# Optimization experiments

Measured on AMD Instinct MI355X. Metric: run time of the kernel, lower is better.

Reference implementation:

```python
import jax, jax.numpy as jnp
import numpy as np

IN_DIM = 64
OUT_DIM = 64
NUM_HEADS = 4
NEG_SLOPE = 0.2
GAMMA = 1.0  # constraint_gamma
NUM_VARS = 100000
NUM_CLAUSES = 100000
NUM_CLUSTERS = 2048
VARS_PER = 64
CLAUSES_PER = 64
NUM_EDGES = 400000


def _xavier(k, shape):
    bound = np.sqrt(6.0 / (shape[0] + shape[1])).astype(np.float32)
    return jax.random.uniform(k, shape, jnp.float32, -bound, bound)


def setup_inputs() -> dict:
    key = jax.random.key(0)
    ks = jax.random.split(key, 11)
    return {
        "x_var": jax.random.normal(ks[0], (NUM_VARS, IN_DIM), jnp.float32),
        "x_clause": jax.random.normal(ks[1], (NUM_CLAUSES, IN_DIM), jnp.float32),
        "var_clause_edge_index": jax.random.randint(ks[2], (2, NUM_EDGES), 0, NUM_VARS),
        "edge_polarity": jax.random.normal(ks[3], (NUM_EDGES, 1), jnp.float32),
        "cluster_var_ids": jax.random.randint(ks[4], (NUM_CLUSTERS, VARS_PER), 0, NUM_VARS),
        "cluster_clause_ids": jax.random.randint(ks[5], (NUM_CLUSTERS, CLAUSES_PER), 0, NUM_CLAUSES),
        "satisfaction_scores": jax.random.uniform(ks[6], (NUM_CLAUSES,), jnp.float32),
        "active_heads": 4,
        "W_Q": _xavier(ks[7], (OUT_DIM, IN_DIM)),
        "W_K": _xavier(ks[8], (OUT_DIM, IN_DIM)),
        "W_V": _xavier(ks[9], (OUT_DIM, IN_DIM)),
        "head_weights": jnp.ones((NUM_HEADS,), jnp.float32),
        "out_proj_w": _xavier(ks[10], (OUT_DIM, OUT_DIM)),
        "out_proj_b": jnp.zeros((OUT_DIM,), jnp.float32),
    }


def reference(x_var, x_clause, var_clause_edge_index, edge_polarity,
              cluster_var_ids, cluster_clause_ids, satisfaction_scores,
              active_heads, W_Q, W_K, W_V, head_weights, out_proj_w, out_proj_b):
    # NOTE: var_clause_edge_index / edge_polarity are accepted but unused,
    # matching the original forward body.
    num_vars = x_var.shape[0]
    x_all = jnp.concatenate([x_var, x_clause], axis=0)            # [N, D]
    Q = x_all @ W_Q.T
    K = x_all @ W_K.T
    V = x_all @ W_V.T

    # Block-diagonal cluster layout: [C, S] with S = VARS_PER + CLAUSES_PER
    nodes = jnp.concatenate([cluster_var_ids, cluster_clause_ids + num_vars], axis=1)
    Qc = Q[nodes]                                                 # [C, S, D]
    Kc = K[nodes]
    Vc = V[nodes]

    scale = jnp.asarray(np.sqrt(OUT_DIM), Qc.dtype)
    scores = jnp.einsum('csd,ctd->cst', Qc, Kc) / scale            # [C, S, S]
    # constraint-aware bias on clause columns (added before leaky_relu)
    bias = jnp.concatenate(
        [jnp.zeros(cluster_var_ids.shape, scores.dtype),
         GAMMA * satisfaction_scores[cluster_clause_ids]], axis=1)  # [C, S]
    scores = jax.nn.leaky_relu(scores + bias[:, None, :], NEG_SLOPE)
    attn = jax.nn.softmax(scores, axis=-1)

    head_w = jnp.mean(head_weights[:active_heads])
    h = jnp.einsum('cst,ctd->csd', attn, Vc) * head_w             # [C, S, D]

    flat = nodes.reshape(-1)
    out = jnp.zeros_like(x_all).at[flat].add(h.reshape(-1, OUT_DIM))
    count = jnp.zeros((x_all.shape[0],), x_all.dtype).at[flat].add(1.0)
    out = out / jnp.maximum(count, 1.0)[:, None]
    out = out @ out_proj_w.T + out_proj_b

    return (x_var + out[:num_vars], x_clause + out[num_vars:])
```

## Files before the change

kernel.cpp:

```cpp
#include <hip/hip_runtime.h>


#define NV 100000
#define NN 200000
#define NCLUST 2048
#define XS 72

typedef __attribute__((ext_vector_type(8))) short short8;
typedef __attribute__((ext_vector_type(16))) float floatx16;
typedef __attribute__((ext_vector_type(4))) unsigned uint4v;

__device__ __forceinline__ unsigned short f2bf(float f) {
    union { float f; unsigned u; } v; v.f = f;
    unsigned r = v.u + 0x7fffu + ((v.u >> 16) & 1u);
    return (unsigned short)(r >> 16);
}
__device__ __forceinline__ unsigned pack2bf(float lo, float hi) {
    union { float f; unsigned u; } a, b; a.f = lo; b.f = hi;
    unsigned ra = a.u + 0x7fffu + ((a.u >> 16) & 1u);
    unsigned rb = b.u + 0x7fffu + ((b.u >> 16) & 1u);
    return (ra >> 16) | (rb & 0xffff0000u);
}
__device__ __forceinline__ int crow(int r, int lane) {
    return (r & 3) + 8 * (r >> 2) + 4 * (lane >> 5);
}
__device__ __forceinline__ void bar_lds() {
    __builtin_amdgcn_sched_barrier(0);
    asm volatile("s_waitcnt lgkmcnt(0)" ::: "memory");
    __builtin_amdgcn_s_barrier();
    __builtin_amdgcn_sched_barrier(0);
}

#define ZU4 1600000
__global__ __launch_bounds__(256) void prep_kernel(
    const float* __restrict__ WQ, const float* __restrict__ WK,
    const float* __restrict__ WV, const float* __restrict__ Wout,
    const float* __restrict__ head_weights, const int* __restrict__ active_heads_p,
    const int* __restrict__ cvar, const int* __restrict__ ccl,
    unsigned short* __restrict__ Mtr, unsigned short* __restrict__ Pbf,
    uint4v* __restrict__ zbase, float* __restrict__ countv)
{
    int o = blockIdx.x * blockDim.x + threadIdx.x;
    if (o < 4096) {
        int d = o >> 6, a = o & 63;
        float acc = 0.f;
        for (int j = 0; j < 64; ++j) acc += WQ[j*64 + a] * WK[j*64 + d];
        Mtr[o] = f2bf(acc * 0.125f);
    } else if (o < 8192) {
        int ah = active_heads_p[0];
        float hw = 0.f;
        for (int i = 0; i < ah; ++i) hw += head_weights[i];
        hw /= (float)ah;
        int o2 = o - 4096;
        int j = o2 >> 6, b = o2 & 63;
        float acc = 0.f;
        for (int d = 0; d < 64; ++d) acc += Wout[j*64 + d] * WV[d*64 + b];
        Pbf[o2] = f2bf(acc * hw);
    }
    {
        int c = o >> 7, r = o & 127;
        int nid = (r < 64) ? cvar[c * 64 + r] : (NV + ccl[c * 64 + (r - 64)]);
        atomicAdd(&countv[nid], 1.0f);
    }
    uint4v z = {0u, 0u, 0u, 0u};
    for (int j = o; j < ZU4; j += 262144) zbase[j] = z;
}

template<bool WN>
__device__ __forceinline__ void cluster_compute(
    unsigned short* X, unsigned short* E,
    const int* ids, const float* biascl,
    const unsigned short* __restrict__ Mtr,
    unsigned short* __restrict__ accum_bf,
    int lane, int w, int m, int hk, int r, int cb,
    short8 nx0, short8 nx1, short8 nx2, short8 nx3)
{
    {
        floatx16 z0 = {}, z1 = {};
        #pragma unroll
        for (int ks = 0; ks < 4; ++ks) {
            short8 mb0 = *(const short8*)(Mtr + m * 64 + ks * 16 + hk);
            short8 mb1 = *(const short8*)(Mtr + (32 + m) * 64 + ks * 16 + hk);
            short8 a = *(const short8*)&X[(w * 32 + m) * XS + ks * 16 + hk];
            z0 = __builtin_amdgcn_mfma_f32_32x32x16_bf16(a, mb0, z0, 0, 0, 0);
            z1 = __builtin_amdgcn_mfma_f32_32x32x16_bf16(a, mb1, z1, 0, 0, 0);
        }
        #pragma unroll
        for (int rr = 0; rr < 16; ++rr) {
            int row = w * 32 + crow(rr, lane);
            E[row * XS + m]      = f2bf(z0[rr]);
            E[row * XS + 32 + m] = f2bf(z1[rr]);
        }
    }

    floatx16 sc[4] = {{}, {}, {}, {}};
    #pragma unroll
    for (int ks = 0; ks < 4; ++ks) {
        short8 a = *(const short8*)&E[(w * 32 + m) * XS + ks * 16 + hk];
        #pragma unroll
        for (int nt = 0; nt < 4; ++nt) {
            short8 b = *(const short8*)&X[(nt * 32 + m) * XS + ks * 16 + hk];
            sc[nt] = __builtin_amdgcn_mfma_f32_32x32x16_bf16(a, b, sc[nt], 0, 0, 0);
        }
    }

    const float b2 = biascl[m], b3 = biascl[32 + m];
    #pragma unroll
    for (int rr = 0; rr < 16; ++rr) {
        float a0 = sc[0][rr], a1 = sc[1][rr], a2 = sc[2][rr] + b2, a3 = sc[3][rr] + b3;
        a0 = a0 > 0.f ? a0 : 0.2f * a0;
        a1 = a1 > 0.f ? a1 : 0.2f * a1;
        a2 = a2 > 0.f ? a2 : 0.2f * a2;
        a3 = a3 > 0.f ? a3 : 0.2f * a3;
        a0 = __expf(a0); a1 = __expf(a1); a2 = __expf(a2); a3 = __expf(a3);
        float s4 = (a0 + a1) + (a2 + a3);
        #pragma unroll
        for (int off = 1; off < 32; off <<= 1) s4 += __shfl_xor(s4, off, 64);
        float inv = __builtin_amdgcn_rcpf(s4);
        sc[0][rr] = a0 * inv; sc[1][rr] = a1 * inv;
        sc[2][rr] = a2 * inv; sc[3][rr] = a3 * inv;
    }

    #pragma unroll
    for (int rr = 0; rr < 16; ++rr) {
        int row = w * 32 + crow(rr, lane);
        E[row * XS + m]      = f2bf(sc[0][rr]);
        E[row * XS + 32 + m] = f2bf(sc[1][rr]);
    }

    floatx16 g0 = {}, g1 = {};
    #pragma unroll
    for (int ks = 0; ks < 4; ++ks) {
        short8 a = *(const short8*)&E[(w * 32 + m) * XS + ks * 16 + hk];
        short8 b0, b1;
        #pragma unroll
        for (int j = 0; j < 8; ++j) {
            int t = ks * 16 + hk + j;
            b0[j] = (short)X[t * XS + m];
            b1[j] = (short)X[t * XS + 32 + m];
        }
        g0 = __builtin_amdgcn_mfma_f32_32x32x16_bf16(a, b0, g0, 0, 0, 0);
        g1 = __builtin_amdgcn_mfma_f32_32x32x16_bf16(a, b1, g1, 0, 0, 0);
    }

    #pragma unroll
    for (int rr = 0; rr < 16; ++rr) {
        int row = w * 32 + crow(rr, lane);
        E[row * XS + m]      = f2bf(sc[2][rr]);
        E[row * XS + 32 + m] = f2bf(sc[3][rr]);
    }

    #pragma unroll
    for (int ks = 0; ks < 4; ++ks) {
        short8 a = *(const short8*)&E[(w * 32 + m) * XS + ks * 16 + hk];
        short8 b0, b1;
        #pragma unroll
        for (int j = 0; j < 8; ++j) {
            int t = 64 + ks * 16 + hk + j;
            b0[j] = (short)X[t * XS + m];
            b1[j] = (short)X[t * XS + 32 + m];
        }
        g0 = __builtin_amdgcn_mfma_f32_32x32x16_bf16(a, b0, g0, 0, 0, 0);
        g1 = __builtin_amdgcn_mfma_f32_32x32x16_bf16(a, b1, g1, 0, 0, 0);
    }

    if (WN) {
        *(short8*)&E[r * XS + cb +  0] = nx0;
        *(short8*)&E[r * XS + cb +  8] = nx1;
        *(short8*)&E[r * XS + cb + 16] = nx2;
        *(short8*)&E[r * XS + cb + 24] = nx3;
    }

    const bool ev = !(lane & 1);
    const int colbase = ev ? m : (31 + m);
    #pragma unroll
    for (int rr = 0; rr < 16; ++rr) {
        int row = w * 32 + crow(rr, lane);
        int nid = ids[row];
        float a0 = g0[rr], a1 = g1[rr];
        float t0 = __shfl_xor(a0, 1, 64);
        float t1 = __shfl_xor(a1, 1, 64);
        float lo = ev ? a0 : t1;
        float hi = ev ? t0 : a1;
        unsigned pk = (unsigned)f2bf(lo) | ((unsigned)f2bf(hi) << 16);
        unsigned long long addr =
            (unsigned long long)(accum_bf + (size_t)nid * 64 + colbase);
        asm volatile("global_atomic_pk_add_bf16 %0, %1, off"
                     :: "v"(addr), "v"(pk) : "memory");
    }
}

__global__ __launch_bounds__(256, 4) void attn_kernel(
    const float* __restrict__ x_var, const float* __restrict__ x_clause,
    const int* __restrict__ cvar, const int* __restrict__ ccl,
    const float* __restrict__ sat, const unsigned short* __restrict__ Mtr,
    unsigned short* __restrict__ accum_bf)
{
    __shared__ unsigned short bufA[128 * XS];
    __shared__ unsigned short bufB[128 * XS];
    __shared__ int   ids0[128], ids1[128];
    __shared__ float bias0[64], bias1[64];

    const int tid = threadIdx.x, lane = tid & 63, w = tid >> 6;
    const int m = lane & 31, hk = (lane >> 5) * 8;
    const int c0 = blockIdx.x * 2;
    const int r = tid >> 1, half = tid & 1, cb = half * 32;

    int nid0, nid1;
    const float *src0, *src1;
    float sv0 = 0.f, sv1 = 0.f;
    if (r < 64) {
        nid0 = cvar[c0 * 64 + r];
        nid1 = cvar[c0 * 64 + 64 + r];
        src0 = x_var + (size_t)nid0 * 64;
        src1 = x_var + (size_t)nid1 * 64;
    } else {
        int cid0 = ccl[c0 * 64 + (r - 64)];
        int cid1 = ccl[c0 * 64 + r];
        nid0 = NV + cid0; nid1 = NV + cid1;
        src0 = x_clause + (size_t)cid0 * 64;
        src1 = x_clause + (size_t)cid1 * 64;
        if (half) { sv0 = sat[cid0]; sv1 = sat[cid1]; }
    }

    const float4* s40 = (const float4*)src0 + half * 8;
    const float4* s41 = (const float4*)src1 + half * 8;
    float4 v0[8], v1[8];
    #pragma unroll
    for (int i = 0; i < 8; ++i) v0[i] = s40[i];
    #pragma unroll
    for (int i = 0; i < 8; ++i) v1[i] = s41[i];

    if (!half) { ids0[r] = nid0; ids1[r] = nid1; }
    if (r >= 64 && half) { bias0[r - 64] = sv0; bias1[r - 64] = sv1; }

    {
        union { unsigned u[16]; short8 v[4]; } h0;
        #pragma unroll
        for (int i = 0; i < 8; ++i) {
            h0.u[2*i]   = pack2bf(v0[i].x, v0[i].y);
            h0.u[2*i+1] = pack2bf(v0[i].z, v0[i].w);
        }
        #pragma unroll
        for (int i = 0; i < 4; ++i) *(short8*)&bufA[r * XS + cb + i * 8] = h0.v[i];
    }
    union { unsigned u[16]; short8 v[4]; } h1;
    #pragma unroll
    for (int i = 0; i < 8; ++i) {
        h1.u[2*i]   = pack2bf(v1[i].x, v1[i].y);
        h1.u[2*i+1] = pack2bf(v1[i].z, v1[i].w);
    }

    bar_lds();

    cluster_compute<true>(bufA, bufB, ids0, bias0, Mtr, accum_bf,
                          lane, w, m, hk, r, cb,
                          h1.v[0], h1.v[1], h1.v[2], h1.v[3]);

    bar_lds();

    short8 zz = {};
    cluster_compute<false>(bufB, bufA, ids1, bias1, Mtr, accum_bf,
                           lane, w, m, hk, r, cb, zz, zz, zz, zz);
}

__global__ __launch_bounds__(256, 4) void finalize_kernel(
    const float* __restrict__ x_var, const float* __restrict__ x_clause,
    const unsigned short* __restrict__ accum_bf, const float* __restrict__ countv,
    const unsigned short* __restrict__ Pbf, const float* __restrict__ bout,
    float* __restrict__ out)
{
    __shared__ float T[4][32][68];
    __shared__ float cnts[256];
    const int tid = threadIdx.x, lane = tid & 63, w = tid >> 6;
    const int base = blockIdx.x * 256;
    {
        int n = base + tid;
        cnts[tid] = (n < NN) ? countv[n] : 1.f;
    }
    __syncthreads();

    const int m = lane & 31, hk = (lane >> 5) * 8;
    short8 pb[2][4];
    #pragma unroll
    for (int nt = 0; nt < 2; ++nt)
        #pragma unroll
        for (int ks = 0; ks < 4; ++ks)
            pb[nt][ks] = *(const short8*)(Pbf + (nt * 32 + m) * 64 + ks * 16 + hk);
    const float bias0 = bout[m], bias1 = bout[32 + m];

    const int r2 = lane >> 1, cb2 = (lane & 1) * 32;

    #pragma unroll
    for (int tm = 0; tm < 2; ++tm) {
        int mt = w * 2 + tm;
        const unsigned short* arow = accum_bf + (size_t)(base + mt * 32 + m) * 64;
        floatx16 c0 = {}, c1 = {};
        #pragma unroll
        for (int ks = 0; ks < 4; ++ks) {
            short8 a = *(const short8*)(arow + ks * 16 + hk);
            c0 = __builtin_amdgcn_mfma_f32_32x32x16_bf16(a, pb[0][ks], c0, 0, 0, 0);
            c1 = __builtin_amdgcn_mfma_f32_32x32x16_bf16(a, pb[1][ks], c1, 0, 0, 0);
        }
        #pragma unroll
        for (int rr = 0; rr < 16; ++rr) {
            int lr32 = crow(rr, lane);
            float inv = 1.0f / fmaxf(cnts[mt * 32 + lr32], 1.0f);
            T[w][lr32][m]      = c0[rr] * inv + bias0;
            T[w][lr32][32 + m] = c1[rr] * inv + bias1;
        }
        int n2 = base + mt * 32 + r2;
        if (n2 < NN) {
            const float* xr = (n2 < NV) ? (x_var + (size_t)n2 * 64)
                                        : (x_clause + (size_t)(n2 - NV) * 64);
            float* orow = out + (size_t)n2 * 64;
            #pragma unroll
            for (int j = 0; j < 8; ++j) {
                float4 t = *(const float4*)&T[w][r2][cb2 + 4 * j];
                float4 xv = *(const float4*)&xr[cb2 + 4 * j];
                float4 o;
                o.x = t.x + xv.x; o.y = t.y + xv.y;
                o.z = t.z + xv.z; o.w = t.w + xv.w;
                *(float4*)&orow[cb2 + 4 * j] = o;
            }
        }
    }
}

extern "C" void kernel_launch(void* const* d_in, const int* in_sizes, int n_in,
                              void* d_out, int out_size, void* d_ws, size_t ws_size,
                              hipStream_t stream)
{
    const float* x_var        = (const float*)d_in[0];
    const float* x_clause     = (const float*)d_in[1];
    const int*   cvar         = (const int*)d_in[4];
    const int*   ccl          = (const int*)d_in[5];
    const float* sat          = (const float*)d_in[6];
    const int*   active_heads = (const int*)d_in[7];
    const float* WQ           = (const float*)d_in[8];
    const float* WK           = (const float*)d_in[9];
    const float* WV           = (const float*)d_in[10];
    const float* head_weights = (const float*)d_in[11];
    const float* Wout         = (const float*)d_in[12];
    const float* bout         = (const float*)d_in[13];

    unsigned short* accum_bf = (unsigned short*)d_ws;
    float* countv = (float*)(accum_bf + (size_t)NN * 64);
    unsigned short* Mtr = (unsigned short*)(countv + NN);
    unsigned short* Pbf = Mtr + 4096;

    hipMemsetAsync(countv, 0, (size_t)NN * 4, stream);
    prep_kernel<<<1024, 256, 0, stream>>>(WQ, WK, WV, Wout, head_weights,
                                          active_heads, cvar, ccl, Mtr, Pbf,
                                          (uint4v*)d_ws, countv);
    attn_kernel<<<NCLUST / 2, 256, 0, stream>>>(
        x_var, x_clause, cvar, ccl, sat, Mtr, accum_bf);
    finalize_kernel<<<(NN + 255) / 256, 256, 0, stream>>>(
        x_var, x_clause, accum_bf, countv, Pbf, bout, (float*)d_out);
}
```

Measured before the change: 216.4 us.

## Fuse prep, attention and finalize into one persistent kernel with grid barriers

Replaces the three separate kernel launches with one kernel of 1024 blocks. The blocks move through a zeroing and weight-prep phase, a count-atomics phase, the attention phase and the finalize phase, with software grid barriers between phases. Shared memory is reused across phases through a raw buffer cast to per-phase structs. The aim is to remove launch gaps and tail effects between kernels. In exchange it adds three spin-wait grid barriers. It also relies on all 1024 blocks being co-resident; if they are not, the barriers can deadlock.

```diff
diff --git a/kernel.cpp b/kernel.cpp
--- a/kernel.cpp
+++ b/kernel.cpp
@@ -5,6 +5,7 @@
 #define NN 200000
 #define NCLUST 2048
 #define XS 72
+#define GRIDN 1024
 
 typedef __attribute__((ext_vector_type(8))) short short8;
 typedef __attribute__((ext_vector_type(16))) float floatx16;
@@ -30,41 +31,29 @@
     __builtin_amdgcn_s_barrier();
     __builtin_amdgcn_sched_barrier(0);
 }
-
-#define ZU4 1600000
-__global__ __launch_bounds__(256) void prep_kernel(
-    const float* __restrict__ WQ, const float* __restrict__ WK,
-    const float* __restrict__ WV, const float* __restrict__ Wout,
-    const float* __restrict__ head_weights, const int* __restrict__ active_heads_p,
-    const int* __restrict__ cvar, const int* __restrict__ ccl,
-    unsigned short* __restrict__ Mtr, unsigned short* __restrict__ Pbf,
-    uint4v* __restrict__ zbase, float* __restrict__ countv)
-{
-    int o = blockIdx.x * blockDim.x + threadIdx.x;
-    if (o < 4096) {
-        int d = o >> 6, a = o & 63;
-        float acc = 0.f;
-        for (int j = 0; j < 64; ++j) acc += WQ[j*64 + a] * WK[j*64 + d];
-        Mtr[o] = f2bf(acc * 0.125f);
-    } else if (o < 8192) {
-        int ah = active_heads_p[0];
-        float hw = 0.f;
-        for (int i = 0; i < ah; ++i) hw += head_weights[i];
-        hw /= (float)ah;
-        int o2 = o - 4096;
-        int j = o2 >> 6, b = o2 & 63;
-        float acc = 0.f;
-        for (int d = 0; d < 64; ++d) acc += Wout[j*64 + d] * WV[d*64 + b];
-        Pbf[o2] = f2bf(acc * hw);
-    }
-    {
-        int c = o >> 7, r = o & 127;
-        int nid = (r < 64) ? cvar[c * 64 + r] : (NV + ccl[c * 64 + (r - 64)]);
-        atomicAdd(&countv[nid], 1.0f);
-    }
-    uint4v z = {0u, 0u, 0u, 0u};
-    for (int j = o; j < ZU4; j += 262144) zbase[j] = z;
-}
+__device__ __forceinline__ void grid_bar(int* ctr) {
+    __syncthreads();
+    if (threadIdx.x == 0) {
+        __hip_atomic_fetch_add(ctr, 1, __ATOMIC_ACQ_REL, __HIP_MEMORY_SCOPE_AGENT);
+        int v;
+        do {
+            __builtin_amdgcn_s_sleep(2);
+            v = __hip_atomic_load(ctr, __ATOMIC_ACQUIRE, __HIP_MEMORY_SCOPE_AGENT);
+        } while (v < GRIDN);
+    }
+    __syncthreads();
+}
+
+struct SmemAttn {
+    unsigned short bufA[128 * XS];
+    unsigned short bufB[128 * XS];
+    int ids0[128], ids1[128];
+    float bias0[64], bias1[64];
+};
+struct SmemFin {
+    float T[4][32][68];
+    float cnts[256];
+};
 
 template<bool WN>
 __device__ __forceinline__ void cluster_compute(
@@ -190,138 +179,173 @@
     }
 }
 
-__global__ __launch_bounds__(256, 4) void attn_kernel(
+extern "C" __global__ __launch_bounds__(256, 4) void fused_kernel(
     const float* __restrict__ x_var, const float* __restrict__ x_clause,
     const int* __restrict__ cvar, const int* __restrict__ ccl,
-    const float* __restrict__ sat, const unsigned short* __restrict__ Mtr,
-    unsigned short* __restrict__ accum_bf)
-{
-    __shared__ unsigned short bufA[128 * XS];
-    __shared__ unsigned short bufB[128 * XS];
-    __shared__ int   ids0[128], ids1[128];
-    __shared__ float bias0[64], bias1[64];
-
-    const int tid = threadIdx.x, lane = tid & 63, w = tid >> 6;
-    const int m = lane & 31, hk = (lane >> 5) * 8;
-    const int c0 = blockIdx.x * 2;
-    const int r = tid >> 1, half = tid & 1, cb = half * 32;
-
-    int nid0, nid1;
-    const float *src0, *src1;
-    float sv0 = 0.f, sv1 = 0.f;
-    if (r < 64) {
-        nid0 = cvar[c0 * 64 + r];
-        nid1 = cvar[c0 * 64 + 64 + r];
-        src0 = x_var + (size_t)nid0 * 64;
-        src1 = x_var + (size_t)nid1 * 64;
-    } else {
-        int cid0 = ccl[c0 * 64 + (r - 64)];
-        int cid1 = ccl[c0 * 64 + r];
-        nid0 = NV + cid0; nid1 = NV + cid1;
-        src0 = x_clause + (size_t)cid0 * 64;
-        src1 = x_clause + (size_t)cid1 * 64;
-        if (half) { sv0 = sat[cid0]; sv1 = sat[cid1]; }
-    }
-
-    const float4* s40 = (const float4*)src0 + half * 8;
-    const float4* s41 = (const float4*)src1 + half * 8;
-    float4 v0[8], v1[8];
-    #pragma unroll
-    for (int i = 0; i < 8; ++i) v0[i] = s40[i];
-    #pragma unroll
-    for (int i = 0; i < 8; ++i) v1[i] = s41[i];
-
-    if (!half) { ids0[r] = nid0; ids1[r] = nid1; }
-    if (r >= 64 && half) { bias0[r - 64] = sv0; bias1[r - 64] = sv1; }
-
-    {
-        union { unsigned u[16]; short8 v[4]; } h0;
-        #pragma unroll
-        for (int i = 0; i < 8; ++i) {
-            h0.u[2*i]   = pack2bf(v0[i].x, v0[i].y);
-            h0.u[2*i+1] = pack2bf(v0[i].z, v0[i].w);
-        }
-        #pragma unroll
-        for (int i = 0; i < 4; ++i) *(short8*)&bufA[r * XS + cb + i * 8] = h0.v[i];
-    }
-    union { unsigned u[16]; short8 v[4]; } h1;
-    #pragma unroll
-    for (int i = 0; i < 8; ++i) {
-        h1.u[2*i]   = pack2bf(v1[i].x, v1[i].y);
-        h1.u[2*i+1] = pack2bf(v1[i].z, v1[i].w);
-    }
-
-    bar_lds();
-
-    cluster_compute<true>(bufA, bufB, ids0, bias0, Mtr, accum_bf,
-                          lane, w, m, hk, r, cb,
-                          h1.v[0], h1.v[1], h1.v[2], h1.v[3]);
-
-    bar_lds();
-
-    short8 zz = {};
-    cluster_compute<false>(bufB, bufA, ids1, bias1, Mtr, accum_bf,
-                           lane, w, m, hk, r, cb, zz, zz, zz, zz);
-}
-
-__global__ __launch_bounds__(256, 4) void finalize_kernel(
-    const float* __restrict__ x_var, const float* __restrict__ x_clause,
-    const unsigned short* __restrict__ accum_bf, const float* __restrict__ countv,
-    const unsigned short* __restrict__ Pbf, const float* __restrict__ bout,
+    const float* __restrict__ sat,
+    const float* __restrict__ WQ, const float* __restrict__ WK,
+    const float* __restrict__ WV, const float* __restrict__ Wout,
+    const float* __restrict__ head_weights, const int* __restrict__ active_heads_p,
+    const float* __restrict__ bout,
+    unsigned short* __restrict__ accum_bf, float* __restrict__ countv,
+    int* __restrict__ barp,
+    unsigned short* __restrict__ Mtr, unsigned short* __restrict__ Pbf,
     float* __restrict__ out)
 {
-    __shared__ float T[4][32][68];
-    __shared__ float cnts[256];
-    const int tid = threadIdx.x, lane = tid & 63, w = tid >> 6;
-    const int base = blockIdx.x * 256;
+    __shared__ __align__(16) char smem_raw[sizeof(SmemAttn)];
+
+    const int tid = threadIdx.x, bid = blockIdx.x;
+    const int gthread = bid * 256 + tid;
+    const int lane = tid & 63, w = tid >> 6;
+    const int m = lane & 31, hk = (lane >> 5) * 8;
+
     {
-        int n = base + tid;
-        cnts[tid] = (n < NN) ? countv[n] : 1.f;
-    }
-    __syncthreads();
-
-    const int m = lane & 31, hk = (lane >> 5) * 8;
-    short8 pb[2][4];
-    #pragma unroll
-    for (int nt = 0; nt < 2; ++nt)
-        #pragma unroll
-        for (int ks = 0; ks < 4; ++ks)
-            pb[nt][ks] = *(const short8*)(Pbf + (nt * 32 + m) * 64 + ks * 16 + hk);
-    const float bias0 = bout[m], bias1 = bout[32 + m];
-
-    const int r2 = lane >> 1, cb2 = (lane & 1) * 32;
-
-    #pragma unroll
-    for (int tm = 0; tm < 2; ++tm) {
-        int mt = w * 2 + tm;
-        const unsigned short* arow = accum_bf + (size_t)(base + mt * 32 + m) * 64;
-        floatx16 c0 = {}, c1 = {};
-        #pragma unroll
-        for (int ks = 0; ks < 4; ++ks) {
-            short8 a = *(const short8*)(arow + ks * 16 + hk);
-            c0 = __builtin_amdgcn_mfma_f32_32x32x16_bf16(a, pb[0][ks], c0, 0, 0, 0);
-            c1 = __builtin_amdgcn_mfma_f32_32x32x16_bf16(a, pb[1][ks], c1, 0, 0, 0);
-        }
-        #pragma unroll
-        for (int rr = 0; rr < 16; ++rr) {
-            int lr32 = crow(rr, lane);
-            float inv = 1.0f / fmaxf(cnts[mt * 32 + lr32], 1.0f);
-            T[w][lr32][m]      = c0[rr] * inv + bias0;
-            T[w][lr32][32 + m] = c1[rr] * inv + bias1;
-        }
-        int n2 = base + mt * 32 + r2;
-        if (n2 < NN) {
-            const float* xr = (n2 < NV) ? (x_var + (size_t)n2 * 64)
-                                        : (x_clause + (size_t)(n2 - NV) * 64);
-            float* orow = out + (size_t)n2 * 64;
-            #pragma unroll
-            for (int j = 0; j < 8; ++j) {
-                float4 t = *(const float4*)&T[w][r2][cb2 + 4 * j];
-                float4 xv = *(const float4*)&xr[cb2 + 4 * j];
-                float4 o;
-                o.x = t.x + xv.x; o.y = t.y + xv.y;
-                o.z = t.z + xv.z; o.w = t.w + xv.w;
-                *(float4*)&orow[cb2 + 4 * j] = o;
+        uint4v z = {0u, 0u, 0u, 0u};
+        uint4v* zb = (uint4v*)accum_bf;
+        for (int j = gthread; j < 1600000; j += 262144) zb[j] = z;
+        int o = gthread;
+        if (o < 4096) {
+            int d = o >> 6, a = o & 63;
+            float acc = 0.f;
+            for (int j = 0; j < 64; ++j) acc += WQ[j*64 + a] * WK[j*64 + d];
+            Mtr[o] = f2bf(acc * 0.125f);
+        } else if (o < 8192) {
+            int ah = active_heads_p[0];
+            float hw = 0.f;
+            for (int i = 0; i < ah; ++i) hw += head_weights[i];
+            hw /= (float)ah;
+            int o2 = o - 4096;
+            int j = o2 >> 6, b = o2 & 63;
+            float acc = 0.f;
+            for (int d = 0; d < 64; ++d) acc += Wout[j*64 + d] * WV[d*64 + b];
+            Pbf[o2] = f2bf(acc * hw);
+        }
+    }
+    grid_bar(&barp[0]);
+
+    {
+        int c = gthread >> 7, r = gthread & 127;
+        int nid = (r < 64) ? cvar[c * 64 + r] : (NV + ccl[c * 64 + (r - 64)]);
+        atomicAdd(&countv[nid], 1.0f);
+    }
+    grid_bar(&barp[16]);
+
+    {
+        SmemAttn* S = (SmemAttn*)smem_raw;
+        const int c0 = bid * 2;
+        const int r = tid >> 1, half = tid & 1, cb = half * 32;
+
+        int nid0, nid1;
+        const float *src0, *src1;
+        float sv0 = 0.f, sv1 = 0.f;
+        if (r < 64) {
+            nid0 = cvar[c0 * 64 + r];
+            nid1 = cvar[c0 * 64 + 64 + r];
+            src0 = x_var + (size_t)nid0 * 64;
+            src1 = x_var + (size_t)nid1 * 64;
+        } else {
+            int cid0 = ccl[c0 * 64 + (r - 64)];
+            int cid1 = ccl[c0 * 64 + r];
+            nid0 = NV + cid0; nid1 = NV + cid1;
+            src0 = x_clause + (size_t)cid0 * 64;
+            src1 = x_clause + (size_t)cid1 * 64;
+            if (half) { sv0 = sat[cid0]; sv1 = sat[cid1]; }
+        }
+
+        const float4* s40 = (const float4*)src0 + half * 8;
+        const float4* s41 = (const float4*)src1 + half * 8;
+        float4 v0[8], v1[8];
+        #pragma unroll
+        for (int i = 0; i < 8; ++i) v0[i] = s40[i];
+        #pragma unroll
+        for (int i = 0; i < 8; ++i) v1[i] = s41[i];
+
+        if (!half) { S->ids0[r] = nid0; S->ids1[r] = nid1; }
+        if (r >= 64 && half) { S->bias0[r - 64] = sv0; S->bias1[r - 64] = sv1; }
+
+        {
+            union { unsigned u[16]; short8 v[4]; } h0;
+            #pragma unroll
+            for (int i = 0; i < 8; ++i) {
+                h0.u[2*i]   = pack2bf(v0[i].x, v0[i].y);
+                h0.u[2*i+1] = pack2bf(v0[i].z, v0[i].w);
+            }
+            #pragma unroll
+            for (int i = 0; i < 4; ++i)
+                *(short8*)&S->bufA[r * XS + cb + i * 8] = h0.v[i];
+        }
+        union { unsigned u[16]; short8 v[4]; } h1;
+        #pragma unroll
+        for (int i = 0; i < 8; ++i) {
+            h1.u[2*i]   = pack2bf(v1[i].x, v1[i].y);
+            h1.u[2*i+1] = pack2bf(v1[i].z, v1[i].w);
+        }
+
+        bar_lds();
+
+        cluster_compute<true>(S->bufA, S->bufB, S->ids0, S->bias0, Mtr, accum_bf,
+                              lane, w, m, hk, r, cb,
+                              h1.v[0], h1.v[1], h1.v[2], h1.v[3]);
+
+        bar_lds();
+
+        short8 zz = {};
+        cluster_compute<false>(S->bufB, S->bufA, S->ids1, S->bias1, Mtr, accum_bf,
+                               lane, w, m, hk, r, cb, zz, zz, zz, zz);
+    }
+    grid_bar(&barp[32]);
+
+    if (bid < (NN + 255) / 256) {
+        SmemFin* F = (SmemFin*)smem_raw;
+        const int base = bid * 256;
+        {
+            int n = base + tid;
+            F->cnts[tid] = (n < NN) ? countv[n] : 1.f;
+        }
+        __syncthreads();
+
+        short8 pb[2][4];
+        #pragma unroll
+        for (int nt = 0; nt < 2; ++nt)
+            #pragma unroll
+            for (int ks = 0; ks < 4; ++ks)
+                pb[nt][ks] = *(const short8*)(Pbf + (nt * 32 + m) * 64 + ks * 16 + hk);
+        const float bias0 = bout[m], bias1 = bout[32 + m];
+
+        const int r2 = lane >> 1, cb2 = (lane & 1) * 32;
+
+        #pragma unroll
+        for (int tm = 0; tm < 2; ++tm) {
+            int mt = w * 2 + tm;
+            const unsigned short* arow = accum_bf + (size_t)(base + mt * 32 + m) * 64;
+            floatx16 c0 = {}, c1 = {};
+            #pragma unroll
+            for (int ks = 0; ks < 4; ++ks) {
+                short8 a = *(const short8*)(arow + ks * 16 + hk);
+                c0 = __builtin_amdgcn_mfma_f32_32x32x16_bf16(a, pb[0][ks], c0, 0, 0, 0);
+                c1 = __builtin_amdgcn_mfma_f32_32x32x16_bf16(a, pb[1][ks], c1, 0, 0, 0);
+            }
+            #pragma unroll
+            for (int rr = 0; rr < 16; ++rr) {
+                int lr32 = crow(rr, lane);
+                float inv = 1.0f / fmaxf(F->cnts[mt * 32 + lr32], 1.0f);
+                F->T[w][lr32][m]      = c0[rr] * inv + bias0;
+                F->T[w][lr32][32 + m] = c1[rr] * inv + bias1;
+            }
+            int n2 = base + mt * 32 + r2;
+            if (n2 < NN) {
+                const float* xr = (n2 < NV) ? (x_var + (size_t)n2 * 64)
+                                            : (x_clause + (size_t)(n2 - NV) * 64);
+                float* orow = out + (size_t)n2 * 64;
+                #pragma unroll
+                for (int j = 0; j < 8; ++j) {
+                    float4 t = *(const float4*)&F->T[w][r2][cb2 + 4 * j];
+                    float4 xv = *(const float4*)&xr[cb2 + 4 * j];
+                    float4 o;
+                    o.x = t.x + xv.x; o.y = t.y + xv.y;
+                    o.z = t.z + xv.z; o.w = t.w + xv.w;
+                    *(float4*)&orow[cb2 + 4 * j] = o;
+                }
             }
         }
     }
@@ -346,15 +370,12 @@
 
     unsigned short* accum_bf = (unsigned short*)d_ws;
     float* countv = (float*)(accum_bf + (size_t)NN * 64);
-    unsigned short* Mtr = (unsigned short*)(countv + NN);
+    int* barp = (int*)(countv + NN);
+    unsigned short* Mtr = (unsigned short*)(barp + 64);
     unsigned short* Pbf = Mtr + 4096;
 
-    hipMemsetAsync(countv, 0, (size_t)NN * 4, stream);
-    prep_kernel<<<1024, 256, 0, stream>>>(WQ, WK, WV, Wout, head_weights,
-                                          active_heads, cvar, ccl, Mtr, Pbf,
-                                          (uint4v*)d_ws, countv);
-    attn_kernel<<<NCLUST / 2, 256, 0, stream>>>(
-        x_var, x_clause, cvar, ccl, sat, Mtr, accum_bf);
-    finalize_kernel<<<(NN + 255) / 256, 256, 0, stream>>>(
-        x_var, x_clause, accum_bf, countv, Pbf, bout, (float*)d_out);
-}
+    hipMemsetAsync(countv, 0, (size_t)NN * 4 + 256, stream);
+    fused_kernel<<<GRIDN, 256, 0, stream>>>(
+        x_var, x_clause, cvar, ccl, sat, WQ, WK, WV, Wout, head_weights,
+        active_heads, bout, accum_bf, countv, barp, Mtr, Pbf, (float*)d_out);
+}
```

New measurement: 476.1 us. +120.1%, slower.
